# Kernel tuning notes

Hardware: AMD Instinct MI355X
Metric: run time of the kernel (lower is better)

The kernel has to match this reference:

```python
import jax, jax.numpy as jnp
import numpy as np

BN_EPS = 1e-5

def _l2norm(x, axis):
    return x / (1e-6 + jnp.linalg.norm(x, axis=axis, keepdims=True))

def setup_inputs() -> dict:
    key = jax.random.key(0)
    ks = jax.random.split(key, 4)
    c, k = 512, 64
    b, h, w = 16, 64, 64
    x = jax.random.normal(ks[0], (b, c, h, w), dtype=jnp.float32)
    conv1_w = jax.random.normal(ks[1], (c, c), dtype=jnp.float32) * np.sqrt(2.0 / c)
    conv1_b = jnp.zeros((c,), dtype=jnp.float32)
    mu = jax.random.normal(ks[2], (1, c, k), dtype=jnp.float32) * np.sqrt(2.0 / k)
    mu = _l2norm(mu, axis=1)
    conv2_w = jax.random.normal(ks[3], (c, c), dtype=jnp.float32) * np.sqrt(2.0 / c)
    bn_gamma = jnp.ones((c,), dtype=jnp.float32)
    bn_beta = jnp.zeros((c,), dtype=jnp.float32)
    bn_mean = jnp.zeros((c,), dtype=jnp.float32)
    bn_var = jnp.ones((c,), dtype=jnp.float32)
    return {"x": x, "conv1_w": conv1_w, "conv1_b": conv1_b, "mu": mu,
            "conv2_w": conv2_w, "bn_gamma": bn_gamma, "bn_beta": bn_beta,
            "bn_mean": bn_mean, "bn_var": bn_var}

STAGE_NUM = 3

def reference(x, conv1_w, conv1_b, mu, conv2_w, bn_gamma, bn_beta, bn_mean, bn_var):
    idn = x
    b, c, h, w = x.shape
    # conv1: 1x1 conv with bias
    xf = jnp.einsum('oc,bchw->bohw', conv1_w, x) + conv1_b[None, :, None, None]
    xf = xf.reshape(b, c, h * w)            # [b, c, n]
    mu_b = jnp.broadcast_to(mu, (b,) + mu.shape[1:])  # [b, c, k]

    # EM iterations (no-grad in original; here just the forward loop)
    def em_step(mu_b, _):
        z = jnp.einsum('bcn,bck->bnk', xf, mu_b)          # [b, n, k]
        z = jax.nn.softmax(z, axis=2)
        z_ = z / (1e-6 + z.sum(axis=1, keepdims=True))
        mu_new = _l2norm(jnp.einsum('bcn,bnk->bck', xf, z_), axis=1)
        return mu_new, z

    mu_b, zs = jax.lax.scan(em_step, mu_b, None, length=STAGE_NUM)
    z = zs[-1]                                            # last-stage responsibilities
    mu_b = jax.lax.stop_gradient(mu_b)
    z = jax.lax.stop_gradient(z)

    xr = jnp.einsum('bck,bnk->bcn', mu_b, z).reshape(b, c, h, w)
    xr = jax.nn.relu(xr)
    # conv2: 1x1 conv (no bias) + BatchNorm (inference mode)
    xr = jnp.einsum('oc,bchw->bohw', conv2_w, xr)
    inv = bn_gamma / jnp.sqrt(bn_var + BN_EPS)
    xr = xr * inv[None, :, None, None] + (bn_beta - bn_mean * inv)[None, :, None, None]
    return jax.nn.relu(xr + idn)
```

## Files before the change

### kernel.cpp

```cpp
#include <hip/hip_runtime.h>

typedef __bf16 bf16x8 __attribute__((ext_vector_type(8)));
typedef __bf16 bf16x4 __attribute__((ext_vector_type(4)));
typedef float f32x4 __attribute__((ext_vector_type(4)));

constexpr int CC = 512;
constexpr int KK = 64;
constexpr int NN = 4096;
constexpr int BB = 16;

constexpr size_t R1_OFF    = 0;
constexpr size_t R2_OFF    = 16777216;
constexpr size_t Z_OFF     = 33554432;
constexpr size_t ZT_OFF    = 35651584;
constexpr size_t MUACC_OFF = 37748736;
constexpr size_t ZSUM_OFF  = 38273024;
constexpr size_t MUBF_OFF  = 38274048;
constexpr size_t MUTBF_OFF = 38536192;
constexpr size_t W1BF_OFF  = 38798336;
constexpr size_t W2BF_OFF  = 38929408;

__global__ __launch_bounds__(256) void k_cvt(const float* __restrict__ src,
                                             __bf16* __restrict__ dst, int n8) {
    int i = blockIdx.x * 256 + threadIdx.x;
    if (i < n8) {
        const float4* s4 = (const float4*)src;
        float4 a = s4[i * 2], b = s4[i * 2 + 1];
        bf16x8 o;
        o[0] = (__bf16)a.x; o[1] = (__bf16)a.y; o[2] = (__bf16)a.z; o[3] = (__bf16)a.w;
        o[4] = (__bf16)b.x; o[5] = (__bf16)b.y; o[6] = (__bf16)b.z; o[7] = (__bf16)b.w;
        *(bf16x8*)&dst[(size_t)i * 8] = o;
    }
}

__global__ __launch_bounds__(256) void k_mu_bcast_bf(const float* __restrict__ mu_in,
                                                     __bf16* __restrict__ mu_bf,
                                                     __bf16* __restrict__ muT_bf) {
    int idx = blockIdx.x * 256 + threadIdx.x;
    if (idx < CC * KK) {
        int c = idx >> 6, k = idx & 63;
        __bf16 v = (__bf16)mu_in[idx];
        for (int b = 0; b < BB; ++b) {
            mu_bf[(size_t)b * CC * KK + idx] = v;
            muT_bf[((size_t)b * KK + k) * CC + c] = v;
        }
    }
}

__global__ __launch_bounds__(256) void k_xpose_cvt(const float* __restrict__ X,
                                                   __bf16* __restrict__ XT) {
    int n0 = blockIdx.x * 64, c0 = blockIdx.y * 64, b = blockIdx.z;
    __shared__ float T[64][65];
    int tid = threadIdx.x;
    const float* Xb = X + (size_t)b * CC * NN;
#pragma unroll
    for (int p = 0; p < 4; ++p) {
        int f4 = tid + p * 256;
        int row = f4 >> 4, col4 = (f4 & 15) * 4;
        float4 v = *(const float4*)&Xb[(size_t)(c0 + row) * NN + n0 + col4];
        T[row][col4 + 0] = v.x; T[row][col4 + 1] = v.y;
        T[row][col4 + 2] = v.z; T[row][col4 + 3] = v.w;
    }
    __syncthreads();
#pragma unroll
    for (int p = 0; p < 2; ++p) {
        int q = tid + p * 256;
        int nl = q >> 3, c8 = (q & 7) * 8;
        bf16x8 o;
#pragma unroll
        for (int j = 0; j < 8; ++j) o[j] = (__bf16)T[c8 + j][nl];
        *(bf16x8*)&XT[((size_t)b * NN + n0 + nl) * CC + c0 + c8] = o;
    }
}

__global__ __launch_bounds__(256) void k_conv1_mfma(
    const __bf16* __restrict__ XT, const __bf16* __restrict__ W1,
    const float* __restrict__ bias, __bf16* __restrict__ XFT,
    __bf16* __restrict__ XFC) {
    __shared__ __bf16 As[2][128 * 32];
    __shared__ __bf16 Bs[2][128 * 32];
    __shared__ float sbias[128];
    int tid = threadIdx.x;
    int lane = tid & 63, wave = tid >> 6;
    int wm = wave >> 1, wn = wave & 1;
    int o0 = blockIdx.x * 128, n0 = blockIdx.y * 128, b = blockIdx.z;
    const __bf16* Ab = XT + ((size_t)b * NN + n0) * CC;
    const __bf16* Bb = W1 + (size_t)o0 * CC;
    if (tid < 128) sbias[tid] = bias[o0 + tid];

    f32x4 acc[4][4];
#pragma unroll
    for (int i = 0; i < 4; ++i)
#pragma unroll
        for (int j = 0; j < 4; ++j) acc[i][j] = f32x4{0.f, 0.f, 0.f, 0.f};

    int r0 = tid >> 2, k0c = tid & 3;
    int r1 = (tid + 256) >> 2, k1c = tid & 3;
    int w0 = r0 * 32 + (k0c ^ ((r0 >> 1) & 3)) * 8;
    int w1 = r1 * 32 + (k1c ^ ((r1 >> 1) & 3)) * 8;

    bf16x8 va0, va1, vb0, vb1;
    va0 = *(const bf16x8*)(Ab + (size_t)r0 * CC + k0c * 8);
    va1 = *(const bf16x8*)(Ab + (size_t)r1 * CC + k1c * 8);
    vb0 = *(const bf16x8*)(Bb + (size_t)r0 * CC + k0c * 8);
    vb1 = *(const bf16x8*)(Bb + (size_t)r1 * CC + k1c * 8);
    *(bf16x8*)&As[0][w0] = va0; *(bf16x8*)&As[0][w1] = va1;
    *(bf16x8*)&Bs[0][w0] = vb0; *(bf16x8*)&Bs[0][w1] = vb1;
    __syncthreads();

    for (int kt = 0; kt < 16; ++kt) {
        int s = kt & 1;
        if (kt < 15) {
            const __bf16* Ak = Ab + (kt + 1) * 32;
            const __bf16* Bk = Bb + (kt + 1) * 32;
            va0 = *(const bf16x8*)(Ak + (size_t)r0 * CC + k0c * 8);
            va1 = *(const bf16x8*)(Ak + (size_t)r1 * CC + k1c * 8);
            vb0 = *(const bf16x8*)(Bk + (size_t)r0 * CC + k0c * 8);
            vb1 = *(const bf16x8*)(Bk + (size_t)r1 * CC + k1c * 8);
        }
        bf16x8 af[4], bg[4];
#pragma unroll
        for (int f = 0; f < 4; ++f) {
            int ra = wm * 64 + f * 16 + (lane & 15);
            af[f] = *(const bf16x8*)&As[s][ra * 32 + (((lane >> 4) ^ ((ra >> 1) & 3))) * 8];
            int rb = wn * 64 + f * 16 + (lane & 15);
            bg[f] = *(const bf16x8*)&Bs[s][rb * 32 + (((lane >> 4) ^ ((rb >> 1) & 3))) * 8];
        }
#pragma unroll
        for (int i = 0; i < 4; ++i)
#pragma unroll
            for (int j = 0; j < 4; ++j)
                acc[i][j] = __builtin_amdgcn_mfma_f32_16x16x32_bf16(af[i], bg[j], acc[i][j], 0, 0, 0);
        if (kt < 15) {
            *(bf16x8*)&As[s ^ 1][w0] = va0; *(bf16x8*)&As[s ^ 1][w1] = va1;
            *(bf16x8*)&Bs[s ^ 1][w0] = vb0; *(bf16x8*)&Bs[s ^ 1][w1] = vb1;
        }
        __syncthreads();
    }

    int gq = lane >> 4, ln = lane & 15;
#pragma unroll
    for (int mf = 0; mf < 4; ++mf) {
#pragma unroll
        for (int nf = 0; nf < 4; ++nf) {
            int o_loc = wn * 64 + nf * 16 + ln;
            int n_loc4 = wm * 64 + mf * 16 + gq * 4;
            float bi = sbias[o_loc];
            bf16x4 oc;
#pragma unroll
            for (int r = 0; r < 4; ++r) oc[r] = (__bf16)(acc[mf][nf][r] + bi);
            *(bf16x4*)&XFC[((size_t)b * CC + o0 + o_loc) * NN + n0 + n_loc4] = oc;
#pragma unroll
            for (int r = 0; r < 4; ++r) {
                XFT[((size_t)b * NN + n0 + n_loc4 + r) * CC + o0 + o_loc] = oc[r];
            }
        }
    }
}

__global__ __launch_bounds__(256) void k_conv2_mfma(
    const __bf16* __restrict__ W2, const __bf16* __restrict__ XRT,
    const float* __restrict__ gamma, const float* __restrict__ beta,
    const float* __restrict__ mean, const float* __restrict__ var,
    const float* __restrict__ Xres, float* __restrict__ Out) {
    __shared__ __bf16 As[2][128 * 32];
    __shared__ __bf16 Bs[2][128 * 32];
    __shared__ float sp0[128], sp1[128];
    int tid = threadIdx.x;
    int lane = tid & 63, wave = tid >> 6;
    int wm = wave >> 1, wn = wave & 1;
    int n0 = blockIdx.x * 128, m0 = blockIdx.y * 128, b = blockIdx.z;
    const __bf16* Ab = XRT + ((size_t)b * NN + n0) * CC;
    const __bf16* Bb = W2 + (size_t)m0 * CC;
    if (tid < 128) {
        float iv = gamma[m0 + tid] * rsqrtf(var[m0 + tid] + 1e-5f);
        sp0[tid] = iv;
        sp1[tid] = beta[m0 + tid] - mean[m0 + tid] * iv;
    }

    f32x4 acc[4][4];
#pragma unroll
    for (int i = 0; i < 4; ++i)
#pragma unroll
        for (int j = 0; j < 4; ++j) acc[i][j] = f32x4{0.f, 0.f, 0.f, 0.f};

    int r0 = tid >> 2, k0c = tid & 3;
    int r1 = (tid + 256) >> 2, k1c = tid & 3;
    int w0 = r0 * 32 + (k0c ^ ((r0 >> 1) & 3)) * 8;
    int w1 = r1 * 32 + (k1c ^ ((r1 >> 1) & 3)) * 8;

    bf16x8 va0, va1, vb0, vb1;
    va0 = *(const bf16x8*)(Ab + (size_t)r0 * CC + k0c * 8);
    va1 = *(const bf16x8*)(Ab + (size_t)r1 * CC + k1c * 8);
    vb0 = *(const bf16x8*)(Bb + (size_t)r0 * CC + k0c * 8);
    vb1 = *(const bf16x8*)(Bb + (size_t)r1 * CC + k1c * 8);
    *(bf16x8*)&As[0][w0] = va0; *(bf16x8*)&As[0][w1] = va1;
    *(bf16x8*)&Bs[0][w0] = vb0; *(bf16x8*)&Bs[0][w1] = vb1;
    __syncthreads();

    for (int kt = 0; kt < 16; ++kt) {
        int s = kt & 1;
        if (kt < 15) {
            const __bf16* Ak = Ab + (kt + 1) * 32;
            const __bf16* Bk = Bb + (kt + 1) * 32;
            va0 = *(const bf16x8*)(Ak + (size_t)r0 * CC + k0c * 8);
            va1 = *(const bf16x8*)(Ak + (size_t)r1 * CC + k1c * 8);
            vb0 = *(const bf16x8*)(Bk + (size_t)r0 * CC + k0c * 8);
            vb1 = *(const bf16x8*)(Bk + (size_t)r1 * CC + k1c * 8);
        }
        bf16x8 af[4], bg[4];
#pragma unroll
        for (int f = 0; f < 4; ++f) {
            int ra = wm * 64 + f * 16 + (lane & 15);
            af[f] = *(const bf16x8*)&As[s][ra * 32 + (((lane >> 4) ^ ((ra >> 1) & 3))) * 8];
            int rb = wn * 64 + f * 16 + (lane & 15);
            bg[f] = *(const bf16x8*)&Bs[s][rb * 32 + (((lane >> 4) ^ ((rb >> 1) & 3))) * 8];
        }
#pragma unroll
        for (int i = 0; i < 4; ++i)
#pragma unroll
            for (int j = 0; j < 4; ++j)
                acc[i][j] = __builtin_amdgcn_mfma_f32_16x16x32_bf16(af[i], bg[j], acc[i][j], 0, 0, 0);
        if (kt < 15) {
            *(bf16x8*)&As[s ^ 1][w0] = va0; *(bf16x8*)&As[s ^ 1][w1] = va1;
            *(bf16x8*)&Bs[s ^ 1][w0] = vb0; *(bf16x8*)&Bs[s ^ 1][w1] = vb1;
        }
        __syncthreads();
    }

    int gq = lane >> 4, ln = lane & 15;
#pragma unroll
    for (int mf = 0; mf < 4; ++mf) {
#pragma unroll
        for (int nf = 0; nf < 4; ++nf) {
            int o_loc = wn * 64 + nf * 16 + ln;
            int n_loc4 = wm * 64 + mf * 16 + gq * 4;
            size_t addr = ((size_t)b * CC + m0 + o_loc) * NN + n0 + n_loc4;
            float iv = sp0[o_loc], sh = sp1[o_loc];
            float4 xi = *(const float4*)&Xres[addr];
            float4 v;
            v.x = fmaxf(acc[mf][nf][0] * iv + sh + xi.x, 0.f);
            v.y = fmaxf(acc[mf][nf][1] * iv + sh + xi.y, 0.f);
            v.z = fmaxf(acc[mf][nf][2] * iv + sh + xi.z, 0.f);
            v.w = fmaxf(acc[mf][nf][3] * iv + sh + xi.w, 0.f);
            *(float4*)&Out[addr] = v;
        }
    }
}

__global__ __launch_bounds__(256) void k_zsoftmax_mfma(
    const __bf16* __restrict__ XFT, const __bf16* __restrict__ MUT,
    __bf16* __restrict__ Z, __bf16* __restrict__ ZT, float* __restrict__ ZSUM) {
    __shared__ __bf16 As[2][128 * 32];
    __shared__ __bf16 Bs[2][64 * 32];
    __shared__ __bf16 ZL[64][136];
    int tid = threadIdx.x;
    int lane = tid & 63, wave = tid >> 6;
    int n0 = blockIdx.x * 128, b = blockIdx.y;
    const __bf16* Ab = XFT + ((size_t)b * NN + n0) * CC;
    const __bf16* Bb = MUT + (size_t)b * KK * CC;

    f32x4 acc[2][4];
#pragma unroll
    for (int i = 0; i < 2; ++i)
#pragma unroll
        for (int j = 0; j < 4; ++j) acc[i][j] = f32x4{0.f, 0.f, 0.f, 0.f};

    int r0 = tid >> 2, k0c = tid & 3;
    int r1 = (tid + 256) >> 2, k1c = tid & 3;
    int w0 = r0 * 32 + (k0c ^ ((r0 >> 1) & 3)) * 8;
    int w1 = r1 * 32 + (k1c ^ ((r1 >> 1) & 3)) * 8;
    int rB = tid >> 2, kB = tid & 3;
    int wB = rB * 32 + (kB ^ ((rB >> 1) & 3)) * 8;

    bf16x8 va0, va1, vb0;
    va0 = *(const bf16x8*)(Ab + (size_t)r0 * CC + k0c * 8);
    va1 = *(const bf16x8*)(Ab + (size_t)r1 * CC + k1c * 8);
    vb0 = *(const bf16x8*)(Bb + (size_t)rB * CC + kB * 8);
    *(bf16x8*)&As[0][w0] = va0; *(bf16x8*)&As[0][w1] = va1;
    *(bf16x8*)&Bs[0][wB] = vb0;
    __syncthreads();

    for (int kt = 0; kt < 16; ++kt) {
        int s = kt & 1;
        if (kt < 15) {
            const __bf16* Ak = Ab + (kt + 1) * 32;
            const __bf16* Bk = Bb + (kt + 1) * 32;
            va0 = *(const bf16x8*)(Ak + (size_t)r0 * CC + k0c * 8);
            va1 = *(const bf16x8*)(Ak + (size_t)r1 * CC + k1c * 8);
            vb0 = *(const bf16x8*)(Bk + (size_t)rB * CC + kB * 8);
        }
        bf16x8 af[2], bg[4];
#pragma unroll
        for (int f = 0; f < 2; ++f) {
            int ra = wave * 32 + f * 16 + (lane & 15);
            af[f] = *(const bf16x8*)&As[s][ra * 32 + (((lane >> 4) ^ ((ra >> 1) & 3))) * 8];
        }
#pragma unroll
        for (int f = 0; f < 4; ++f) {
            int rb = f * 16 + (lane & 15);
            bg[f] = *(const bf16x8*)&Bs[s][rb * 32 + (((lane >> 4) ^ ((rb >> 1) & 3))) * 8];
        }
#pragma unroll
        for (int i = 0; i < 2; ++i)
#pragma unroll
            for (int j = 0; j < 4; ++j)
                acc[i][j] = __builtin_amdgcn_mfma_f32_16x16x32_bf16(af[i], bg[j], acc[i][j], 0, 0, 0);
        if (kt < 15) {
            *(bf16x8*)&As[s ^ 1][w0] = va0; *(bf16x8*)&As[s ^ 1][w1] = va1;
            *(bf16x8*)&Bs[s ^ 1][wB] = vb0;
        }
        __syncthreads();
    }

    int gq = lane >> 4, ln = lane & 15;
    float zp[4] = {0.f, 0.f, 0.f, 0.f};
#pragma unroll
    for (int mf = 0; mf < 2; ++mf) {
#pragma unroll
        for (int r = 0; r < 4; ++r) {
            float mx = fmaxf(fmaxf(acc[mf][0][r], acc[mf][1][r]),
                             fmaxf(acc[mf][2][r], acc[mf][3][r]));
            mx = fmaxf(mx, __shfl_xor(mx, 1));
            mx = fmaxf(mx, __shfl_xor(mx, 2));
            mx = fmaxf(mx, __shfl_xor(mx, 4));
            mx = fmaxf(mx, __shfl_xor(mx, 8));
            float e[4];
            float ssum = 0.f;
#pragma unroll
            for (int nf = 0; nf < 4; ++nf) { e[nf] = expf(acc[mf][nf][r] - mx); ssum += e[nf]; }
            ssum += __shfl_xor(ssum, 1);
            ssum += __shfl_xor(ssum, 2);
            ssum += __shfl_xor(ssum, 4);
            ssum += __shfl_xor(ssum, 8);
            float inv = 1.0f / ssum;
            int n_loc = wave * 32 + mf * 16 + gq * 4 + r;
            size_t zrow = ((size_t)b * NN + n0 + n_loc) * KK;
#pragma unroll
            for (int nf = 0; nf < 4; ++nf) {
                float zv = e[nf] * inv;
                zp[nf] += zv;
                int k = nf * 16 + ln;
                __bf16 zb = (__bf16)zv;
                Z[zrow + k] = zb;
                ZL[k][n_loc] = zb;
            }
        }
    }
#pragma unroll
    for (int nf = 0; nf < 4; ++nf) {
        float t = zp[nf];
        t += __shfl_xor(t, 16);
        t += __shfl_xor(t, 32);
        if (lane < 16) atomicAdd(&ZSUM[b * KK + nf * 16 + ln], t);
    }
    __syncthreads();
#pragma unroll
    for (int p = 0; p < 4; ++p) {
        int ci = tid + p * 256;
        int kr = ci >> 4, ch = (ci & 15) * 8;
        bf16x8 v = *(const bf16x8*)&ZL[kr][ch];
        *(bf16x8*)&ZT[((size_t)b * KK + kr) * NN + n0 + ch] = v;
    }
}

__global__ __launch_bounds__(256) void k_muacc_mfma(
    const __bf16* __restrict__ XFC, const __bf16* __restrict__ ZT,
    float* __restrict__ MUACC) {
    __shared__ __bf16 As[2][128 * 32];
    __shared__ __bf16 Bs[2][64 * 32];
    int tid = threadIdx.x;
    int lane = tid & 63, wave = tid >> 6;
    int wm = wave >> 1, wn = wave & 1;
    int c0 = (blockIdx.x & 3) * 128, sp = blockIdx.x >> 2, b = blockIdx.y;
    size_t nbase = (size_t)sp * 512;
    const __bf16* Ab = XFC + ((size_t)b * CC + c0) * NN + nbase;
    const __bf16* Bb = ZT + (size_t)b * KK * NN + nbase;

    f32x4 acc[4][2];
#pragma unroll
    for (int i = 0; i < 4; ++i)
#pragma unroll
        for (int j = 0; j < 2; ++j) acc[i][j] = f32x4{0.f, 0.f, 0.f, 0.f};

    int r0 = tid >> 2, k0c = tid & 3;
    int r1 = (tid + 256) >> 2, k1c = tid & 3;
    int w0 = r0 * 32 + (k0c ^ ((r0 >> 1) & 3)) * 8;
    int w1 = r1 * 32 + (k1c ^ ((r1 >> 1) & 3)) * 8;
    int rB = tid >> 2, kB = tid & 3;
    int wB = rB * 32 + (kB ^ ((rB >> 1) & 3)) * 8;

    bf16x8 va0, va1, vb0;
    va0 = *(const bf16x8*)(Ab + (size_t)r0 * NN + k0c * 8);
    va1 = *(const bf16x8*)(Ab + (size_t)r1 * NN + k1c * 8);
    vb0 = *(const bf16x8*)(Bb + (size_t)rB * NN + kB * 8);
    *(bf16x8*)&As[0][w0] = va0; *(bf16x8*)&As[0][w1] = va1;
    *(bf16x8*)&Bs[0][wB] = vb0;
    __syncthreads();

    for (int kt = 0; kt < 16; ++kt) {
        int s = kt & 1;
        if (kt < 15) {
            const __bf16* Ak = Ab + (kt + 1) * 32;
            const __bf16* Bk = Bb + (kt + 1) * 32;
            va0 = *(const bf16x8*)(Ak + (size_t)r0 * NN + k0c * 8);
            va1 = *(const bf16x8*)(Ak + (size_t)r1 * NN + k1c * 8);
            vb0 = *(const bf16x8*)(Bk + (size_t)rB * NN + kB * 8);
        }
        bf16x8 af[4], bg[2];
#pragma unroll
        for (int f = 0; f < 4; ++f) {
            int ra = wm * 64 + f * 16 + (lane & 15);
            af[f] = *(const bf16x8*)&As[s][ra * 32 + (((lane >> 4) ^ ((ra >> 1) & 3))) * 8];
        }
#pragma unroll
        for (int f = 0; f < 2; ++f) {
            int rb = wn * 32 + f * 16 + (lane & 15);
            bg[f] = *(const bf16x8*)&Bs[s][rb * 32 + (((lane >> 4) ^ ((rb >> 1) & 3))) * 8];
        }
#pragma unroll
        for (int i = 0; i < 4; ++i)
#pragma unroll
            for (int j = 0; j < 2; ++j)
                acc[i][j] = __builtin_amdgcn_mfma_f32_16x16x32_bf16(af[i], bg[j], acc[i][j], 0, 0, 0);
        if (kt < 15) {
            *(bf16x8*)&As[s ^ 1][w0] = va0; *(bf16x8*)&As[s ^ 1][w1] = va1;
            *(bf16x8*)&Bs[s ^ 1][wB] = vb0;
        }
        __syncthreads();
    }

    int gq = lane >> 4, ln = lane & 15;
#pragma unroll
    for (int mf = 0; mf < 4; ++mf) {
#pragma unroll
        for (int r = 0; r < 4; ++r) {
            int row = wm * 64 + mf * 16 + gq * 4 + r;
#pragma unroll
            for (int nf = 0; nf < 2; ++nf) {
                int col = wn * 32 + nf * 16 + ln;
                atomicAdd(&MUACC[((size_t)b * CC + c0 + row) * KK + col], acc[mf][nf][r]);
            }
        }
    }
}

__global__ __launch_bounds__(64) void k_munorm_bf(
    const float* __restrict__ MUACC, const float* __restrict__ ZSUM,
    __bf16* __restrict__ mu_bf, __bf16* __restrict__ muT_bf) {
    int k = blockIdx.x;
    int b = blockIdx.y;
    int lane = threadIdx.x;
    float scale = 1.0f / (1e-6f + ZSUM[b * KK + k]);
    float v[8];
    float ss = 0.f;
#pragma unroll
    for (int i = 0; i < 8; ++i) {
        v[i] = MUACC[(size_t)b * CC * KK + (size_t)(lane + i * 64) * KK + k] * scale;
        ss += v[i] * v[i];
    }
    for (int off = 32; off; off >>= 1) ss += __shfl_xor(ss, off);
    float nrm = 1.0f / (1e-6f + sqrtf(ss));
#pragma unroll
    for (int i = 0; i < 8; ++i) {
        int c = lane + i * 64;
        __bf16 o = (__bf16)(v[i] * nrm);
        mu_bf[((size_t)b * CC + c) * KK + k] = o;
        muT_bf[((size_t)b * KK + k) * CC + c] = o;
    }
}

__global__ __launch_bounds__(256) void k_xr_mfma(
    const __bf16* __restrict__ Zm, const __bf16* __restrict__ MUB,
    __bf16* __restrict__ XRT) {
    __shared__ __bf16 As[128 * 64];
    __shared__ __bf16 Bs[128 * 64];
    int tid = threadIdx.x;
    int lane = tid & 63, wave = tid >> 6;
    int wm = wave >> 1, wn = wave & 1;
    int n0 = blockIdx.x * 128, c0 = blockIdx.y * 128, b = blockIdx.z;
    const __bf16* Ab = Zm + ((size_t)b * NN + n0) * KK;
    const __bf16* Bb = MUB + ((size_t)b * CC + c0) * KK;
#pragma unroll
    for (int p = 0; p < 4; ++p) {
        int idx = tid + p * 256;
        int r = idx >> 3, ch = idx & 7;
        int woff = r * 64 + ((ch ^ (r & 7)) * 8);
        *(bf16x8*)&As[woff] = *(const bf16x8*)(Ab + (size_t)r * KK + ch * 8);
        *(bf16x8*)&Bs[woff] = *(const bf16x8*)(Bb + (size_t)r * KK + ch * 8);
    }
    __syncthreads();

    f32x4 acc[4][4];
#pragma unroll
    for (int i = 0; i < 4; ++i)
#pragma unroll
        for (int j = 0; j < 4; ++j) acc[i][j] = f32x4{0.f, 0.f, 0.f, 0.f};

    int gq = lane >> 4, ln = lane & 15;
#pragma unroll
    for (int ks = 0; ks < 2; ++ks) {
        bf16x8 af[4], bg[4];
#pragma unroll
        for (int f = 0; f < 4; ++f) {
            int ra = wm * 64 + f * 16 + ln;
            af[f] = *(const bf16x8*)&As[ra * 64 + (((ks * 4 + gq) ^ (ra & 7))) * 8];
            int rb = wn * 64 + f * 16 + ln;
            bg[f] = *(const bf16x8*)&Bs[rb * 64 + (((ks * 4 + gq) ^ (rb & 7))) * 8];
        }
#pragma unroll
        for (int i = 0; i < 4; ++i)
#pragma unroll
            for (int j = 0; j < 4; ++j)
                acc[i][j] = __builtin_amdgcn_mfma_f32_16x16x32_bf16(af[i], bg[j], acc[i][j], 0, 0, 0);
    }

#pragma unroll
    for (int mf = 0; mf < 4; ++mf) {
#pragma unroll
        for (int r = 0; r < 4; ++r) {
            int n_loc = wm * 64 + mf * 16 + gq * 4 + r;
            size_t orow = ((size_t)b * NN + n0 + n_loc) * CC + c0 + wn * 64;
#pragma unroll
            for (int nf = 0; nf < 4; ++nf) {
                XRT[orow + nf * 16 + ln] = (__bf16)fmaxf(acc[mf][nf][r], 0.f);
            }
        }
    }
}

extern "C" void kernel_launch(void* const* d_in, const int* in_sizes, int n_in,
                              void* d_out, int out_size, void* d_ws, size_t ws_size,
                              hipStream_t stream) {
    const float* x     = (const float*)d_in[0];
    const float* w1    = (const float*)d_in[1];
    const float* b1    = (const float*)d_in[2];
    const float* mu_in = (const float*)d_in[3];
    const float* w2    = (const float*)d_in[4];
    const float* gamma = (const float*)d_in[5];
    const float* beta  = (const float*)d_in[6];
    const float* mean  = (const float*)d_in[7];
    const float* var   = (const float*)d_in[8];
    float* out = (float*)d_out;
    float* ws  = (float*)d_ws;

    __bf16* xt    = (__bf16*)(ws + R1_OFF);
    __bf16* xft   = (__bf16*)(ws + R2_OFF);
    __bf16* xrt   = (__bf16*)(ws + R2_OFF);
    __bf16* xfc   = (__bf16*)d_out;
    __bf16* zbf   = (__bf16*)(ws + Z_OFF);
    __bf16* ztbf  = (__bf16*)(ws + ZT_OFF);
    float*  muacc = ws + MUACC_OFF;
    float*  zsum  = ws + ZSUM_OFF;
    __bf16* mu_bf = (__bf16*)(ws + MUBF_OFF);
    __bf16* muT_bf= (__bf16*)(ws + MUTBF_OFF);
    __bf16* w1bf  = (__bf16*)(ws + W1BF_OFF);
    __bf16* w2bf  = (__bf16*)(ws + W2BF_OFF);

    hipLaunchKernelGGL(k_cvt, dim3(128), dim3(256), 0, stream, w1, w1bf, CC * CC / 8);
    hipLaunchKernelGGL(k_cvt, dim3(128), dim3(256), 0, stream, w2, w2bf, CC * CC / 8);
    hipLaunchKernelGGL(k_mu_bcast_bf, dim3(128), dim3(256), 0, stream, mu_in, mu_bf, muT_bf);
    hipLaunchKernelGGL(k_xpose_cvt, dim3(NN / 64, CC / 64, BB), dim3(256), 0, stream, x, xt);
    hipLaunchKernelGGL(k_conv1_mfma, dim3(CC / 128, NN / 128, BB), dim3(256), 0, stream,
                       xt, w1bf, b1, xft, xfc);
    for (int it = 0; it < 3; ++it) {
        hipMemsetAsync(muacc, 0, (size_t)(BB * CC * KK + BB * KK) * sizeof(float), stream);
        hipLaunchKernelGGL(k_zsoftmax_mfma, dim3(NN / 128, BB), dim3(256), 0, stream,
                           xft, muT_bf, zbf, ztbf, zsum);
        hipLaunchKernelGGL(k_muacc_mfma, dim3(32, BB), dim3(256), 0, stream, xfc, ztbf, muacc);
        hipLaunchKernelGGL(k_munorm_bf, dim3(KK, BB), dim3(64), 0, stream, muacc, zsum,
                           mu_bf, muT_bf);
    }
    hipLaunchKernelGGL(k_xr_mfma, dim3(NN / 128, CC / 128, BB), dim3(256), 0, stream,
                       zbf, mu_bf, xrt);
    hipLaunchKernelGGL(k_conv2_mfma, dim3(NN / 128, CC / 128, BB), dim3(256), 0, stream,
                       w2bf, xrt, gamma, beta, mean, var, x, out);
}
```

Measured before the change: 446.2 us.

## Fuse EM softmax and mu accumulation, stage transposed stores through shared memory

Merges the z-softmax and mu-accumulation kernels into one EM kernel. It reuses the LDS-resident z tile for a per-block partial XFC·z product, accumulated into MUACC with atomics. This drops the ZT round-trip through global memory and writes Z only on the last iteration. Conv1 and xr epilogues now stage their transposed outputs in shared memory so they can issue coalesced 16-byte stores instead of scattered 2-byte stores. The cost is many more fp32 atomics, since each of the 32 n-blocks per batch atomically adds its full 512x64 partial, and XFC fragments are read straight from global memory without LDS staging.

Result: slower. 502.5 us (+12.6%).

```diff
diff --git a/kernel.cpp b/kernel.cpp
--- a/kernel.cpp
+++ b/kernel.cpp
@@ -12,7 +12,6 @@
 constexpr size_t R1_OFF    = 0;
 constexpr size_t R2_OFF    = 16777216;
 constexpr size_t Z_OFF     = 33554432;
-constexpr size_t ZT_OFF    = 35651584;
 constexpr size_t MUACC_OFF = 37748736;
 constexpr size_t ZSUM_OFF  = 38273024;
 constexpr size_t MUBF_OFF  = 38274048;
@@ -77,9 +76,10 @@
     const __bf16* __restrict__ XT, const __bf16* __restrict__ W1,
     const float* __restrict__ bias, __bf16* __restrict__ XFT,
     __bf16* __restrict__ XFC) {
-    __shared__ __bf16 As[2][128 * 32];
-    __shared__ __bf16 Bs[2][128 * 32];
+    __shared__ __bf16 SM[17408];
     __shared__ float sbias[128];
+    __bf16* As = SM;
+    __bf16* Bs = SM + 8192;
     int tid = threadIdx.x;
     int lane = tid & 63, wave = tid >> 6;
     int wm = wave >> 1, wn = wave & 1;
@@ -104,8 +104,8 @@
     va1 = *(const bf16x8*)(Ab + (size_t)r1 * CC + k1c * 8);
     vb0 = *(const bf16x8*)(Bb + (size_t)r0 * CC + k0c * 8);
     vb1 = *(const bf16x8*)(Bb + (size_t)r1 * CC + k1c * 8);
-    *(bf16x8*)&As[0][w0] = va0; *(bf16x8*)&As[0][w1] = va1;
-    *(bf16x8*)&Bs[0][w0] = vb0; *(bf16x8*)&Bs[0][w1] = vb1;
+    *(bf16x8*)&As[w0] = va0; *(bf16x8*)&As[w1] = va1;
+    *(bf16x8*)&Bs[w0] = vb0; *(bf16x8*)&Bs[w1] = vb1;
     __syncthreads();
 
     for (int kt = 0; kt < 16; ++kt) {
@@ -122,9 +122,9 @@
 #pragma unroll
         for (int f = 0; f < 4; ++f) {
             int ra = wm * 64 + f * 16 + (lane & 15);
-            af[f] = *(const bf16x8*)&As[s][ra * 32 + (((lane >> 4) ^ ((ra >> 1) & 3))) * 8];
+            af[f] = *(const bf16x8*)&As[s * 4096 + ra * 32 + (((lane >> 4) ^ ((ra >> 1) & 3))) * 8];
             int rb = wn * 64 + f * 16 + (lane & 15);
-            bg[f] = *(const bf16x8*)&Bs[s][rb * 32 + (((lane >> 4) ^ ((rb >> 1) & 3))) * 8];
+            bg[f] = *(const bf16x8*)&Bs[s * 4096 + rb * 32 + (((lane >> 4) ^ ((rb >> 1) & 3))) * 8];
         }
 #pragma unroll
         for (int i = 0; i < 4; ++i)
@@ -132,12 +132,13 @@
             for (int j = 0; j < 4; ++j)
                 acc[i][j] = __builtin_amdgcn_mfma_f32_16x16x32_bf16(af[i], bg[j], acc[i][j], 0, 0, 0);
         if (kt < 15) {
-            *(bf16x8*)&As[s ^ 1][w0] = va0; *(bf16x8*)&As[s ^ 1][w1] = va1;
-            *(bf16x8*)&Bs[s ^ 1][w0] = vb0; *(bf16x8*)&Bs[s ^ 1][w1] = vb1;
+            *(bf16x8*)&As[(s ^ 1) * 4096 + w0] = va0; *(bf16x8*)&As[(s ^ 1) * 4096 + w1] = va1;
+            *(bf16x8*)&Bs[(s ^ 1) * 4096 + w0] = vb0; *(bf16x8*)&Bs[(s ^ 1) * 4096 + w1] = vb1;
         }
         __syncthreads();
     }
 
+    __bf16* TT = SM;
     int gq = lane >> 4, ln = lane & 15;
 #pragma unroll
     for (int mf = 0; mf < 4; ++mf) {
@@ -151,10 +152,16 @@
             for (int r = 0; r < 4; ++r) oc[r] = (__bf16)(acc[mf][nf][r] + bi);
             *(bf16x4*)&XFC[((size_t)b * CC + o0 + o_loc) * NN + n0 + n_loc4] = oc;
 #pragma unroll
-            for (int r = 0; r < 4; ++r) {
-                XFT[((size_t)b * NN + n0 + n_loc4 + r) * CC + o0 + o_loc] = oc[r];
-            }
-        }
+            for (int r = 0; r < 4; ++r) TT[(n_loc4 + r) * 136 + o_loc] = oc[r];
+        }
+    }
+    __syncthreads();
+#pragma unroll
+    for (int p = 0; p < 8; ++p) {
+        int idx = tid + p * 256;
+        int row = idx >> 4, ch = idx & 15;
+        bf16x8 v = *(const bf16x8*)&TT[row * 136 + ch * 8];
+        *(bf16x8*)&XFT[((size_t)b * NN + n0 + row) * CC + o0 + ch * 8] = v;
     }
 }
 
@@ -248,12 +255,14 @@
     }
 }
 
-__global__ __launch_bounds__(256) void k_zsoftmax_mfma(
+__global__ __launch_bounds__(256) void k_em_fused(
     const __bf16* __restrict__ XFT, const __bf16* __restrict__ MUT,
-    __bf16* __restrict__ Z, __bf16* __restrict__ ZT, float* __restrict__ ZSUM) {
-    __shared__ __bf16 As[2][128 * 32];
-    __shared__ __bf16 Bs[2][64 * 32];
-    __shared__ __bf16 ZL[64][136];
+    const __bf16* __restrict__ XFC, __bf16* __restrict__ Z,
+    float* __restrict__ ZSUM, float* __restrict__ MUACC, int write_z) {
+    __shared__ __bf16 SM[20992];
+    __bf16* As = SM;
+    __bf16* Bs = SM + 8192;
+    __bf16* ZL = SM + 12288;
     int tid = threadIdx.x;
     int lane = tid & 63, wave = tid >> 6;
     int n0 = blockIdx.x * 128, b = blockIdx.y;
@@ -277,8 +286,8 @@
     va0 = *(const bf16x8*)(Ab + (size_t)r0 * CC + k0c * 8);
     va1 = *(const bf16x8*)(Ab + (size_t)r1 * CC + k1c * 8);
     vb0 = *(const bf16x8*)(Bb + (size_t)rB * CC + kB * 8);
-    *(bf16x8*)&As[0][w0] = va0; *(bf16x8*)&As[0][w1] = va1;
-    *(bf16x8*)&Bs[0][wB] = vb0;
+    *(bf16x8*)&As[w0] = va0; *(bf16x8*)&As[w1] = va1;
+    *(bf16x8*)&Bs[wB] = vb0;
     __syncthreads();
 
     for (int kt = 0; kt < 16; ++kt) {
@@ -294,12 +303,12 @@
 #pragma unroll
         for (int f = 0; f < 2; ++f) {
             int ra = wave * 32 + f * 16 + (lane & 15);
-            af[f] = *(const bf16x8*)&As[s][ra * 32 + (((lane >> 4) ^ ((ra >> 1) & 3))) * 8];
+            af[f] = *(const bf16x8*)&As[s * 4096 + ra * 32 + (((lane >> 4) ^ ((ra >> 1) & 3))) * 8];
         }
 #pragma unroll
         for (int f = 0; f < 4; ++f) {
             int rb = f * 16 + (lane & 15);
-            bg[f] = *(const bf16x8*)&Bs[s][rb * 32 + (((lane >> 4) ^ ((rb >> 1) & 3))) * 8];
+            bg[f] = *(const bf16x8*)&Bs[s * 2048 + rb * 32 + (((lane >> 4) ^ ((rb >> 1) & 3))) * 8];
         }
 #pragma unroll
         for (int i = 0; i < 2; ++i)
@@ -307,8 +316,8 @@
             for (int j = 0; j < 4; ++j)
                 acc[i][j] = __builtin_amdgcn_mfma_f32_16x16x32_bf16(af[i], bg[j], acc[i][j], 0, 0, 0);
         if (kt < 15) {
-            *(bf16x8*)&As[s ^ 1][w0] = va0; *(bf16x8*)&As[s ^ 1][w1] = va1;
-            *(bf16x8*)&Bs[s ^ 1][wB] = vb0;
+            *(bf16x8*)&As[(s ^ 1) * 4096 + w0] = va0; *(bf16x8*)&As[(s ^ 1) * 4096 + w1] = va1;
+            *(bf16x8*)&Bs[(s ^ 1) * 2048 + wB] = vb0;
         }
         __syncthreads();
     }
@@ -335,15 +344,11 @@
             ssum += __shfl_xor(ssum, 8);
             float inv = 1.0f / ssum;
             int n_loc = wave * 32 + mf * 16 + gq * 4 + r;
-            size_t zrow = ((size_t)b * NN + n0 + n_loc) * KK;
 #pragma unroll
             for (int nf = 0; nf < 4; ++nf) {
                 float zv = e[nf] * inv;
                 zp[nf] += zv;
-                int k = nf * 16 + ln;
-                __bf16 zb = (__bf16)zv;
-                Z[zrow + k] = zb;
-                ZL[k][n_loc] = zb;
+                ZL[(nf * 16 + ln) * 136 + n_loc] = (__bf16)zv;
             }
         }
     }
@@ -355,91 +360,61 @@
         if (lane < 16) atomicAdd(&ZSUM[b * KK + nf * 16 + ln], t);
     }
     __syncthreads();
-#pragma unroll
-    for (int p = 0; p < 4; ++p) {
-        int ci = tid + p * 256;
-        int kr = ci >> 4, ch = (ci & 15) * 8;
-        bf16x8 v = *(const bf16x8*)&ZL[kr][ch];
-        *(bf16x8*)&ZT[((size_t)b * KK + kr) * NN + n0 + ch] = v;
-    }
-}
-
-__global__ __launch_bounds__(256) void k_muacc_mfma(
-    const __bf16* __restrict__ XFC, const __bf16* __restrict__ ZT,
-    float* __restrict__ MUACC) {
-    __shared__ __bf16 As[2][128 * 32];
-    __shared__ __bf16 Bs[2][64 * 32];
-    int tid = threadIdx.x;
-    int lane = tid & 63, wave = tid >> 6;
-    int wm = wave >> 1, wn = wave & 1;
-    int c0 = (blockIdx.x & 3) * 128, sp = blockIdx.x >> 2, b = blockIdx.y;
-    size_t nbase = (size_t)sp * 512;
-    const __bf16* Ab = XFC + ((size_t)b * CC + c0) * NN + nbase;
-    const __bf16* Bb = ZT + (size_t)b * KK * NN + nbase;
-
-    f32x4 acc[4][2];
-#pragma unroll
-    for (int i = 0; i < 4; ++i)
-#pragma unroll
-        for (int j = 0; j < 2; ++j) acc[i][j] = f32x4{0.f, 0.f, 0.f, 0.f};
-
-    int r0 = tid >> 2, k0c = tid & 3;
-    int r1 = (tid + 256) >> 2, k1c = tid & 3;
-    int w0 = r0 * 32 + (k0c ^ ((r0 >> 1) & 3)) * 8;
-    int w1 = r1 * 32 + (k1c ^ ((r1 >> 1) & 3)) * 8;
-    int rB = tid >> 2, kB = tid & 3;
-    int wB = rB * 32 + (kB ^ ((rB >> 1) & 3)) * 8;
-
-    bf16x8 va0, va1, vb0;
-    va0 = *(const bf16x8*)(Ab + (size_t)r0 * NN + k0c * 8);
-    va1 = *(const bf16x8*)(Ab + (size_t)r1 * NN + k1c * 8);
-    vb0 = *(const bf16x8*)(Bb + (size_t)rB * NN + kB * 8);
-    *(bf16x8*)&As[0][w0] = va0; *(bf16x8*)&As[0][w1] = va1;
-    *(bf16x8*)&Bs[0][wB] = vb0;
-    __syncthreads();
-
-    for (int kt = 0; kt < 16; ++kt) {
-        int s = kt & 1;
-        if (kt < 15) {
-            const __bf16* Ak = Ab + (kt + 1) * 32;
-            const __bf16* Bk = Bb + (kt + 1) * 32;
-            va0 = *(const bf16x8*)(Ak + (size_t)r0 * NN + k0c * 8);
-            va1 = *(const bf16x8*)(Ak + (size_t)r1 * NN + k1c * 8);
-            vb0 = *(const bf16x8*)(Bk + (size_t)rB * NN + kB * 8);
-        }
-        bf16x8 af[4], bg[2];
-#pragma unroll
-        for (int f = 0; f < 4; ++f) {
-            int ra = wm * 64 + f * 16 + (lane & 15);
-            af[f] = *(const bf16x8*)&As[s][ra * 32 + (((lane >> 4) ^ ((ra >> 1) & 3))) * 8];
-        }
-#pragma unroll
-        for (int f = 0; f < 2; ++f) {
-            int rb = wn * 32 + f * 16 + (lane & 15);
-            bg[f] = *(const bf16x8*)&Bs[s][rb * 32 + (((lane >> 4) ^ ((rb >> 1) & 3))) * 8];
-        }
-#pragma unroll
-        for (int i = 0; i < 4; ++i)
-#pragma unroll
-            for (int j = 0; j < 2; ++j)
-                acc[i][j] = __builtin_amdgcn_mfma_f32_16x16x32_bf16(af[i], bg[j], acc[i][j], 0, 0, 0);
-        if (kt < 15) {
-            *(bf16x8*)&As[s ^ 1][w0] = va0; *(bf16x8*)&As[s ^ 1][w1] = va1;
-            *(bf16x8*)&Bs[s ^ 1][wB] = vb0;
-        }
-        __syncthreads();
-    }
-
-    int gq = lane >> 4, ln = lane & 15;
-#pragma unroll
-    for (int mf = 0; mf < 4; ++mf) {
-#pragma unroll
-        for (int r = 0; r < 4; ++r) {
-            int row = wm * 64 + mf * 16 + gq * 4 + r;
-#pragma unroll
-            for (int nf = 0; nf < 2; ++nf) {
-                int col = wn * 32 + nf * 16 + ln;
-                atomicAdd(&MUACC[((size_t)b * CC + c0 + row) * KK + col], acc[mf][nf][r]);
+
+    if (write_z) {
+#pragma unroll
+        for (int p = 0; p < 4; ++p) {
+            int idx = tid + p * 256;
+            int row = idx >> 3, k8 = (idx & 7) * 8;
+            bf16x8 o;
+#pragma unroll
+            for (int j = 0; j < 8; ++j) o[j] = ZL[(k8 + j) * 136 + row];
+            *(bf16x8*)&Z[((size_t)b * NN + n0 + row) * KK + k8] = o;
+        }
+    }
+
+    int wc = wave >> 1, wk = wave & 1;
+    bf16x8 bgh[2][4];
+#pragma unroll
+    for (int f = 0; f < 2; ++f)
+#pragma unroll
+        for (int ks = 0; ks < 4; ++ks)
+            bgh[f][ks] = *(const bf16x8*)&ZL[(wk * 32 + f * 16 + (lane & 15)) * 136 +
+                                            (ks * 4 + (lane >> 4)) * 8];
+
+    for (int cc = 0; cc < 8; ++cc) {
+        int ccr = (cc + blockIdx.x) & 7;
+        const __bf16* Ac = XFC + ((size_t)b * CC + ccr * 64 + wc * 32) * NN + n0;
+        bf16x8 afl[2][4];
+#pragma unroll
+        for (int f = 0; f < 2; ++f)
+#pragma unroll
+            for (int ks = 0; ks < 4; ++ks)
+                afl[f][ks] = *(const bf16x8*)(Ac + (size_t)(f * 16 + (lane & 15)) * NN +
+                                              (ks * 4 + (lane >> 4)) * 8);
+        f32x4 acc2[2][2];
+#pragma unroll
+        for (int i = 0; i < 2; ++i)
+#pragma unroll
+            for (int j = 0; j < 2; ++j) acc2[i][j] = f32x4{0.f, 0.f, 0.f, 0.f};
+#pragma unroll
+        for (int ks = 0; ks < 4; ++ks)
+#pragma unroll
+            for (int i = 0; i < 2; ++i)
+#pragma unroll
+                for (int j = 0; j < 2; ++j)
+                    acc2[i][j] = __builtin_amdgcn_mfma_f32_16x16x32_bf16(
+                        afl[i][ks], bgh[j][ks], acc2[i][j], 0, 0, 0);
+#pragma unroll
+        for (int i = 0; i < 2; ++i) {
+#pragma unroll
+            for (int r = 0; r < 4; ++r) {
+                int c = ccr * 64 + wc * 32 + i * 16 + gq * 4 + r;
+#pragma unroll
+                for (int j = 0; j < 2; ++j) {
+                    int k = wk * 32 + j * 16 + ln;
+                    atomicAdd(&MUACC[((size_t)b * CC + c) * KK + k], acc2[i][j][r]);
+                }
             }
         }
     }
@@ -473,8 +448,9 @@
 __global__ __launch_bounds__(256) void k_xr_mfma(
     const __bf16* __restrict__ Zm, const __bf16* __restrict__ MUB,
     __bf16* __restrict__ XRT) {
-    __shared__ __bf16 As[128 * 64];
-    __shared__ __bf16 Bs[128 * 64];
+    __shared__ __bf16 SM[17408];
+    __bf16* As = SM;
+    __bf16* Bs = SM + 8192;
     int tid = threadIdx.x;
     int lane = tid & 63, wave = tid >> 6;
     int wm = wave >> 1, wn = wave & 1;
@@ -514,18 +490,27 @@
             for (int j = 0; j < 4; ++j)
                 acc[i][j] = __builtin_amdgcn_mfma_f32_16x16x32_bf16(af[i], bg[j], acc[i][j], 0, 0, 0);
     }
-
+    __syncthreads();
+
+    __bf16* TT = SM;
 #pragma unroll
     for (int mf = 0; mf < 4; ++mf) {
 #pragma unroll
-        for (int r = 0; r < 4; ++r) {
-            int n_loc = wm * 64 + mf * 16 + gq * 4 + r;
-            size_t orow = ((size_t)b * NN + n0 + n_loc) * CC + c0 + wn * 64;
-#pragma unroll
-            for (int nf = 0; nf < 4; ++nf) {
-                XRT[orow + nf * 16 + ln] = (__bf16)fmaxf(acc[mf][nf][r], 0.f);
-            }
-        }
+        for (int nf = 0; nf < 4; ++nf) {
+            int c_loc = wn * 64 + nf * 16 + ln;
+            int n_loc4 = wm * 64 + mf * 16 + gq * 4;
+#pragma unroll
+            for (int r = 0; r < 4; ++r)
+                TT[(n_loc4 + r) * 136 + c_loc] = (__bf16)fmaxf(acc[mf][nf][r], 0.f);
+        }
+    }
+    __syncthreads();
+#pragma unroll
+    for (int p = 0; p < 8; ++p) {
+        int idx = tid + p * 256;
+        int row = idx >> 4, ch = idx & 15;
+        bf16x8 v = *(const bf16x8*)&TT[row * 136 + ch * 8];
+        *(bf16x8*)&XRT[((size_t)b * NN + n0 + row) * CC + c0 + ch * 8] = v;
     }
 }
 
@@ -549,7 +534,6 @@
     __bf16* xrt   = (__bf16*)(ws + R2_OFF);
     __bf16* xfc   = (__bf16*)d_out;
     __bf16* zbf   = (__bf16*)(ws + Z_OFF);
-    __bf16* ztbf  = (__bf16*)(ws + ZT_OFF);
     float*  muacc = ws + MUACC_OFF;
     float*  zsum  = ws + ZSUM_OFF;
     __bf16* mu_bf = (__bf16*)(ws + MUBF_OFF);
@@ -565,9 +549,8 @@
                        xt, w1bf, b1, xft, xfc);
     for (int it = 0; it < 3; ++it) {
         hipMemsetAsync(muacc, 0, (size_t)(BB * CC * KK + BB * KK) * sizeof(float), stream);
-        hipLaunchKernelGGL(k_zsoftmax_mfma, dim3(NN / 128, BB), dim3(256), 0, stream,
-                           xft, muT_bf, zbf, ztbf, zsum);
-        hipLaunchKernelGGL(k_muacc_mfma, dim3(32, BB), dim3(256), 0, stream, xfc, ztbf, muacc);
+        hipLaunchKernelGGL(k_em_fused, dim3(NN / 128, BB), dim3(256), 0, stream,
+                           xft, muT_bf, xfc, zbf, zsum, muacc, (it == 2) ? 1 : 0);
         hipLaunchKernelGGL(k_munorm_bf, dim3(KK, BB), dim3(64), 0, stream, muacc, zsum,
                            mu_bf, muT_bf);
     }
```

## Stage transposed epilogue stores through LDS and skip unused Z writes

Applied to the files above, without the earlier changes.

The conv1 and xr epilogues now stage their transposed bf16 outputs in a padded shared-memory tile, then write them as coalesced 16-byte rows instead of scattered 2-byte stores. The softmax kernel writes the row-major Z only on the last EM iteration, since earlier copies are never read, and builds it as vectorised writes from the LDS tile. conv2 prefetches its fp32 residual tile into registers before the GEMM loop so the load can overlap the compute. The cost is extra LDS traffic and barriers, plus higher register pressure in conv2 that may reduce occupancy.

Measured after the change: 430.2 us. 3.6% less time.

```diff
diff --git a/kernel.cpp b/kernel.cpp
--- a/kernel.cpp
+++ b/kernel.cpp
@@ -77,9 +77,10 @@
     const __bf16* __restrict__ XT, const __bf16* __restrict__ W1,
     const float* __restrict__ bias, __bf16* __restrict__ XFT,
     __bf16* __restrict__ XFC) {
-    __shared__ __bf16 As[2][128 * 32];
-    __shared__ __bf16 Bs[2][128 * 32];
+    __shared__ __bf16 SM[17408];
     __shared__ float sbias[128];
+    __bf16* As = SM;
+    __bf16* Bs = SM + 8192;
     int tid = threadIdx.x;
     int lane = tid & 63, wave = tid >> 6;
     int wm = wave >> 1, wn = wave & 1;
@@ -104,8 +105,8 @@
     va1 = *(const bf16x8*)(Ab + (size_t)r1 * CC + k1c * 8);
     vb0 = *(const bf16x8*)(Bb + (size_t)r0 * CC + k0c * 8);
     vb1 = *(const bf16x8*)(Bb + (size_t)r1 * CC + k1c * 8);
-    *(bf16x8*)&As[0][w0] = va0; *(bf16x8*)&As[0][w1] = va1;
-    *(bf16x8*)&Bs[0][w0] = vb0; *(bf16x8*)&Bs[0][w1] = vb1;
+    *(bf16x8*)&As[w0] = va0; *(bf16x8*)&As[w1] = va1;
+    *(bf16x8*)&Bs[w0] = vb0; *(bf16x8*)&Bs[w1] = vb1;
     __syncthreads();
 
     for (int kt = 0; kt < 16; ++kt) {
@@ -122,9 +123,9 @@
 #pragma unroll
         for (int f = 0; f < 4; ++f) {
             int ra = wm * 64 + f * 16 + (lane & 15);
-            af[f] = *(const bf16x8*)&As[s][ra * 32 + (((lane >> 4) ^ ((ra >> 1) & 3))) * 8];
+            af[f] = *(const bf16x8*)&As[s * 4096 + ra * 32 + (((lane >> 4) ^ ((ra >> 1) & 3))) * 8];
             int rb = wn * 64 + f * 16 + (lane & 15);
-            bg[f] = *(const bf16x8*)&Bs[s][rb * 32 + (((lane >> 4) ^ ((rb >> 1) & 3))) * 8];
+            bg[f] = *(const bf16x8*)&Bs[s * 4096 + rb * 32 + (((lane >> 4) ^ ((rb >> 1) & 3))) * 8];
         }
 #pragma unroll
         for (int i = 0; i < 4; ++i)
@@ -132,12 +133,13 @@
             for (int j = 0; j < 4; ++j)
                 acc[i][j] = __builtin_amdgcn_mfma_f32_16x16x32_bf16(af[i], bg[j], acc[i][j], 0, 0, 0);
         if (kt < 15) {
-            *(bf16x8*)&As[s ^ 1][w0] = va0; *(bf16x8*)&As[s ^ 1][w1] = va1;
-            *(bf16x8*)&Bs[s ^ 1][w0] = vb0; *(bf16x8*)&Bs[s ^ 1][w1] = vb1;
+            *(bf16x8*)&As[(s ^ 1) * 4096 + w0] = va0; *(bf16x8*)&As[(s ^ 1) * 4096 + w1] = va1;
+            *(bf16x8*)&Bs[(s ^ 1) * 4096 + w0] = vb0; *(bf16x8*)&Bs[(s ^ 1) * 4096 + w1] = vb1;
         }
         __syncthreads();
     }
 
+    __bf16* TT = SM;
     int gq = lane >> 4, ln = lane & 15;
 #pragma unroll
     for (int mf = 0; mf < 4; ++mf) {
@@ -151,10 +153,16 @@
             for (int r = 0; r < 4; ++r) oc[r] = (__bf16)(acc[mf][nf][r] + bi);
             *(bf16x4*)&XFC[((size_t)b * CC + o0 + o_loc) * NN + n0 + n_loc4] = oc;
 #pragma unroll
-            for (int r = 0; r < 4; ++r) {
-                XFT[((size_t)b * NN + n0 + n_loc4 + r) * CC + o0 + o_loc] = oc[r];
-            }
-        }
+            for (int r = 0; r < 4; ++r) TT[(n_loc4 + r) * 136 + o_loc] = oc[r];
+        }
+    }
+    __syncthreads();
+#pragma unroll
+    for (int p = 0; p < 8; ++p) {
+        int idx = tid + p * 256;
+        int row = idx >> 4, ch = idx & 15;
+        bf16x8 v = *(const bf16x8*)&TT[row * 136 + ch * 8];
+        *(bf16x8*)&XFT[((size_t)b * NN + n0 + row) * CC + o0 + ch * 8] = v;
     }
 }
 
@@ -172,11 +180,22 @@
     int n0 = blockIdx.x * 128, m0 = blockIdx.y * 128, b = blockIdx.z;
     const __bf16* Ab = XRT + ((size_t)b * NN + n0) * CC;
     const __bf16* Bb = W2 + (size_t)m0 * CC;
+    int gq = lane >> 4, ln = lane & 15;
     if (tid < 128) {
         float iv = gamma[m0 + tid] * rsqrtf(var[m0 + tid] + 1e-5f);
         sp0[tid] = iv;
         sp1[tid] = beta[m0 + tid] - mean[m0 + tid] * iv;
     }
+
+    f32x4 xpre[4][4];
+#pragma unroll
+    for (int mf = 0; mf < 4; ++mf)
+#pragma unroll
+        for (int nf = 0; nf < 4; ++nf) {
+            int o_loc = wn * 64 + nf * 16 + ln;
+            int n_loc4 = wm * 64 + mf * 16 + gq * 4;
+            xpre[mf][nf] = *(const f32x4*)&Xres[((size_t)b * CC + m0 + o_loc) * NN + n0 + n_loc4];
+        }
 
     f32x4 acc[4][4];
 #pragma unroll
@@ -228,7 +247,6 @@
         __syncthreads();
     }
 
-    int gq = lane >> 4, ln = lane & 15;
 #pragma unroll
     for (int mf = 0; mf < 4; ++mf) {
 #pragma unroll
@@ -237,12 +255,12 @@
             int n_loc4 = wm * 64 + mf * 16 + gq * 4;
             size_t addr = ((size_t)b * CC + m0 + o_loc) * NN + n0 + n_loc4;
             float iv = sp0[o_loc], sh = sp1[o_loc];
-            float4 xi = *(const float4*)&Xres[addr];
+            f32x4 xi = xpre[mf][nf];
             float4 v;
-            v.x = fmaxf(acc[mf][nf][0] * iv + sh + xi.x, 0.f);
-            v.y = fmaxf(acc[mf][nf][1] * iv + sh + xi.y, 0.f);
-            v.z = fmaxf(acc[mf][nf][2] * iv + sh + xi.z, 0.f);
-            v.w = fmaxf(acc[mf][nf][3] * iv + sh + xi.w, 0.f);
+            v.x = fmaxf(acc[mf][nf][0] * iv + sh + xi[0], 0.f);
+            v.y = fmaxf(acc[mf][nf][1] * iv + sh + xi[1], 0.f);
+            v.z = fmaxf(acc[mf][nf][2] * iv + sh + xi[2], 0.f);
+            v.w = fmaxf(acc[mf][nf][3] * iv + sh + xi[3], 0.f);
             *(float4*)&Out[addr] = v;
         }
     }
@@ -250,7 +268,8 @@
 
 __global__ __launch_bounds__(256) void k_zsoftmax_mfma(
     const __bf16* __restrict__ XFT, const __bf16* __restrict__ MUT,
-    __bf16* __restrict__ Z, __bf16* __restrict__ ZT, float* __restrict__ ZSUM) {
+    __bf16* __restrict__ Z, __bf16* __restrict__ ZT, float* __restrict__ ZSUM,
+    int write_z) {
     __shared__ __bf16 As[2][128 * 32];
     __shared__ __bf16 Bs[2][64 * 32];
     __shared__ __bf16 ZL[64][136];
@@ -335,15 +354,11 @@
             ssum += __shfl_xor(ssum, 8);
             float inv = 1.0f / ssum;
             int n_loc = wave * 32 + mf * 16 + gq * 4 + r;
-            size_t zrow = ((size_t)b * NN + n0 + n_loc) * KK;
 #pragma unroll
             for (int nf = 0; nf < 4; ++nf) {
                 float zv = e[nf] * inv;
                 zp[nf] += zv;
-                int k = nf * 16 + ln;
-                __bf16 zb = (__bf16)zv;
-                Z[zrow + k] = zb;
-                ZL[k][n_loc] = zb;
+                ZL[nf * 16 + ln][n_loc] = (__bf16)zv;
             }
         }
     }
@@ -361,6 +376,17 @@
         int kr = ci >> 4, ch = (ci & 15) * 8;
         bf16x8 v = *(const bf16x8*)&ZL[kr][ch];
         *(bf16x8*)&ZT[((size_t)b * KK + kr) * NN + n0 + ch] = v;
+    }
+    if (write_z) {
+#pragma unroll
+        for (int p = 0; p < 4; ++p) {
+            int idx = tid + p * 256;
+            int row = idx >> 3, k8 = (idx & 7) * 8;
+            bf16x8 o;
+#pragma unroll
+            for (int j = 0; j < 8; ++j) o[j] = ZL[k8 + j][row];
+            *(bf16x8*)&Z[((size_t)b * NN + n0 + row) * KK + k8] = o;
+        }
     }
 }
 
@@ -473,8 +499,9 @@
 __global__ __launch_bounds__(256) void k_xr_mfma(
     const __bf16* __restrict__ Zm, const __bf16* __restrict__ MUB,
     __bf16* __restrict__ XRT) {
-    __shared__ __bf16 As[128 * 64];
-    __shared__ __bf16 Bs[128 * 64];
+    __shared__ __bf16 SM[17408];
+    __bf16* As = SM;
+    __bf16* Bs = SM + 8192;
     int tid = threadIdx.x;
     int lane = tid & 63, wave = tid >> 6;
     int wm = wave >> 1, wn = wave & 1;
@@ -514,18 +541,27 @@
             for (int j = 0; j < 4; ++j)
                 acc[i][j] = __builtin_amdgcn_mfma_f32_16x16x32_bf16(af[i], bg[j], acc[i][j], 0, 0, 0);
     }
-
+    __syncthreads();
+
+    __bf16* TT = SM;
 #pragma unroll
     for (int mf = 0; mf < 4; ++mf) {
 #pragma unroll
-        for (int r = 0; r < 4; ++r) {
-            int n_loc = wm * 64 + mf * 16 + gq * 4 + r;
-            size_t orow = ((size_t)b * NN + n0 + n_loc) * CC + c0 + wn * 64;
-#pragma unroll
-            for (int nf = 0; nf < 4; ++nf) {
-                XRT[orow + nf * 16 + ln] = (__bf16)fmaxf(acc[mf][nf][r], 0.f);
-            }
-        }
+        for (int nf = 0; nf < 4; ++nf) {
+            int c_loc = wn * 64 + nf * 16 + ln;
+            int n_loc4 = wm * 64 + mf * 16 + gq * 4;
+#pragma unroll
+            for (int r = 0; r < 4; ++r)
+                TT[(n_loc4 + r) * 136 + c_loc] = (__bf16)fmaxf(acc[mf][nf][r], 0.f);
+        }
+    }
+    __syncthreads();
+#pragma unroll
+    for (int p = 0; p < 8; ++p) {
+        int idx = tid + p * 256;
+        int row = idx >> 4, ch = idx & 15;
+        bf16x8 v = *(const bf16x8*)&TT[row * 136 + ch * 8];
+        *(bf16x8*)&XRT[((size_t)b * NN + n0 + row) * CC + c0 + ch * 8] = v;
     }
 }
 
@@ -566,7 +602,7 @@
     for (int it = 0; it < 3; ++it) {
         hipMemsetAsync(muacc, 0, (size_t)(BB * CC * KK + BB * KK) * sizeof(float), stream);
         hipLaunchKernelGGL(k_zsoftmax_mfma, dim3(NN / 128, BB), dim3(256), 0, stream,
-                           xft, muT_bf, zbf, ztbf, zsum);
+                           xft, muT_bf, zbf, ztbf, zsum, (it == 2) ? 1 : 0);
         hipLaunchKernelGGL(k_muacc_mfma, dim3(32, BB), dim3(256), 0, stream, xfc, ztbf, muacc);
         hipLaunchKernelGGL(k_munorm_bf, dim3(KK, BB), dim3(64), 0, stream, muacc, zsum,
                            mu_bf, muT_bf);
```
